# Performance work log

Measured on AMD Instinct MI355X. Metric: run time of the kernel, lower is better.

## Reference

```python
import jax, jax.numpy as jnp
import numpy as np

N = 100000          # nodes
E = 1600000         # edges (avg degree 16)
IN_DIM = 128
OUT_DIM = 128
H = 4               # num_heads
D = OUT_DIM // H    # per-head dim = 32
R = 64              # num relations
NEG_SLOPE = 0.2     # DGL GATConv default


def setup_inputs() -> dict:
    key = jax.random.key(0)
    ks = jax.random.split(key, 9)
    h = jax.random.normal(ks[0], (N, IN_DIM), dtype=jnp.float32)
    src = jax.random.randint(ks[1], (E,), 0, N, dtype=jnp.int32)
    dst = jax.random.randint(ks[2], (E,), 0, N, dtype=jnp.int32)
    rel_types = jax.random.randint(ks[3], (E,), 0, R, dtype=jnp.int32)
    # learned params (GATConv fc weight, attention vectors, bias; relation embedding)
    W = jax.random.normal(ks[4], (H * D, IN_DIM), dtype=jnp.float32) * 0.1
    attn_l = jax.random.normal(ks[5], (H, D), dtype=jnp.float32) * 0.1
    attn_r = jax.random.normal(ks[6], (H, D), dtype=jnp.float32) * 0.1
    bias = jax.random.normal(ks[7], (H * D,), dtype=jnp.float32) * 0.01
    rel_emb = jax.random.normal(ks[8], (R, IN_DIM), dtype=jnp.float32) * 0.1
    return {"h": h, "src": src, "dst": dst, "rel_types": rel_types,
            "W": W, "attn_l": attn_l, "attn_r": attn_r, "bias": bias,
            "rel_emb": rel_emb}


def reference(h, src, dst, rel_types, W, attn_l, attn_r, bias, rel_emb):
    # NOTE: the original module builds edata 'e' = h[src] + rel_emb[rel_types],
    # but DGL's GATConv never reads it, so it does not affect the output.
    # Eval mode: feat_drop / attn_drop disabled (deterministic reference).

    # GATConv: project and split heads. [N, H, D]
    feat = (h @ W.T).reshape(N, H, D)
    # per-node attention logits: a_l^T Wh_i, a_r^T Wh_j  -> [N, H]
    el = (feat * attn_l).sum(-1)
    er = (feat * attn_r).sum(-1)
    # per-edge score e_ij = LeakyReLU(el[src] + er[dst])  -> [E, H]
    e = jax.nn.leaky_relu(el[src] + er[dst], NEG_SLOPE)
    # segment softmax over incoming edges of each destination node
    m = jax.ops.segment_max(e, dst, num_segments=N)           # [N, H]
    a = jnp.exp(e - m[dst])                                    # [E, H]
    denom = jax.ops.segment_sum(a, dst, num_segments=N)       # [N, H]
    alpha = a / denom[dst]                                     # [E, H]
    # weighted scatter-aggregate of source features
    msg = feat[src] * alpha[:, :, None]                        # [E, H, D]
    out = jax.ops.segment_sum(msg, dst, num_segments=N)       # [N, H, D]
    out = out + bias.reshape(1, H, D)
    # mean over heads -> [N, D]
    return out.mean(axis=1)
```

## Files before the change

### kernel.cpp

```cpp
#include <hip/hip_runtime.h>
#include <hip/hip_bf16.h>
#include <math.h>

#define NEG_SLOPE 0.2f

__device__ __forceinline__ float bf2f(unsigned int hw) {
    return __uint_as_float(hw << 16);
}
__device__ __forceinline__ unsigned short f2bf(float f) {
    unsigned int u = __float_as_uint(f);
    u += 0x7FFFu + ((u >> 16) & 1u);
    return (unsigned short)(u >> 16);
}

__global__ __launch_bounds__(256, 3) void k_gemm(const float* __restrict__ h,
                                                 const float* __restrict__ W,
                                                 unsigned short* __restrict__ featp,
                                                 int N) {
    __shared__ float As[64 * 68];
    __shared__ float Bs[128 * 64];
    const int tid = threadIdx.x;
    const int rb = blockIdx.x * 64;
    const int tc = tid & 31;
    const int tr = tid >> 5;

    float acc[8][4];
#pragma unroll
    for (int i = 0; i < 8; ++i)
#pragma unroll
        for (int j = 0; j < 4; ++j) acc[i][j] = 0.0f;

    for (int kch = 0; kch < 2; ++kch) {
        if (kch) __syncthreads();
#pragma unroll
        for (int i = 0; i < 4; ++i) {
            int chunk = i * 256 + tid;
            int r = chunk >> 4;
            int kc = (chunk & 15) << 2;
            int row = rb + r;
            float4 v = make_float4(0.f, 0.f, 0.f, 0.f);
            if (row < N) v = *(const float4*)(h + (size_t)row * 128 + kch * 64 + kc);
            *(float4*)(As + r * 68 + kc) = v;
        }
#pragma unroll
        for (int i = 0; i < 8; ++i) {
            int chunk = i * 256 + tid;
            int c = chunk >> 4;
            int kc = (chunk & 15) << 2;
            float4 v = *(const float4*)(W + (size_t)c * 128 + kch * 64 + kc);
            int slot = (kc >> 2) ^ (c & 7);
            *(float4*)(Bs + (c << 6) + (slot << 2)) = v;
        }
        __syncthreads();

#pragma unroll 4
        for (int k4 = 0; k4 < 64; k4 += 4) {
            float4 b[4];
#pragma unroll
            for (int j = 0; j < 4; ++j) {
                int c = tc + 32 * j;
                int slot = (k4 >> 2) ^ (c & 7);
                b[j] = *(const float4*)(Bs + (c << 6) + (slot << 2));
            }
            float4 a[8];
#pragma unroll
            for (int i = 0; i < 8; ++i)
                a[i] = *(const float4*)(As + (tr * 8 + i) * 68 + k4);
#pragma unroll
            for (int i = 0; i < 8; ++i)
#pragma unroll
                for (int j = 0; j < 4; ++j)
                    acc[i][j] += a[i].x * b[j].x + a[i].y * b[j].y +
                                 a[i].z * b[j].z + a[i].w * b[j].w;
        }
    }
#pragma unroll
    for (int i = 0; i < 8; ++i) {
        int row = rb + tr * 8 + i;
        if (row < N) {
            ushort4 pk;
            pk.x = f2bf(acc[i][0]);
            pk.y = f2bf(acc[i][1]);
            pk.z = f2bf(acc[i][2]);
            pk.w = f2bf(acc[i][3]);
            *(ushort4*)(featp + (size_t)row * 128 + tc * 4) = pk;
        }
    }
}

__global__ void k_elr(const unsigned short* __restrict__ featp,
                      const float* __restrict__ attn_l,
                      const float* __restrict__ attn_r,
                      float* __restrict__ el, float* __restrict__ er, int N) {
    int g = blockIdx.x * blockDim.x + threadIdx.x;
    int node = g >> 5;
    int d = g & 31;
    if (node >= N) return;
    uint2 u = *(const uint2*)(featp + (size_t)node * 128 + d * 4);
    float f0 = bf2f(u.x & 0xffffu);
    float f1 = bf2f(u.x >> 16);
    float f2 = bf2f(u.y & 0xffffu);
    float f3 = bf2f(u.y >> 16);
    float pl0 = f0 * attn_l[d],      pr0 = f0 * attn_r[d];
    float pl1 = f1 * attn_l[32 + d], pr1 = f1 * attn_r[32 + d];
    float pl2 = f2 * attn_l[64 + d], pr2 = f2 * attn_r[64 + d];
    float pl3 = f3 * attn_l[96 + d], pr3 = f3 * attn_r[96 + d];
#pragma unroll
    for (int m = 1; m < 32; m <<= 1) {
        pl0 += __shfl_xor(pl0, m); pr0 += __shfl_xor(pr0, m);
        pl1 += __shfl_xor(pl1, m); pr1 += __shfl_xor(pr1, m);
        pl2 += __shfl_xor(pl2, m); pr2 += __shfl_xor(pr2, m);
        pl3 += __shfl_xor(pl3, m); pr3 += __shfl_xor(pr3, m);
    }
    if (d == 0) {
        *(float4*)(el + (size_t)node * 4) = make_float4(pl0, pl1, pl2, pl3);
        *(float4*)(er + (size_t)node * 4) = make_float4(pr0, pr1, pr2, pr3);
    }
}

__global__ void k_hist(const int* __restrict__ dst, int* __restrict__ cnt,
                       int* __restrict__ pos, int E) {
    int e = blockIdx.x * blockDim.x + threadIdx.x;
    if (e < E) pos[e] = atomicAdd(&cnt[dst[e]], 1);
}

__global__ void k_scan1(const int* __restrict__ cnt, int* __restrict__ bsum, int N) {
    __shared__ int sd[256];
    int t = threadIdx.x;
    int i = blockIdx.x * 256 + t;
    sd[t] = (i < N) ? cnt[i] : 0;
    __syncthreads();
    for (int s = 128; s > 0; s >>= 1) {
        if (t < s) sd[t] += sd[t + s];
        __syncthreads();
    }
    if (t == 0) bsum[blockIdx.x] = sd[0];
}

__global__ void k_scan2(int* __restrict__ bsum, int nb) {
    __shared__ int sd[1024];
    int t = threadIdx.x;
    sd[t] = (t < nb) ? bsum[t] : 0;
    __syncthreads();
    for (int off = 1; off < 1024; off <<= 1) {
        int add = (t >= off) ? sd[t - off] : 0;
        __syncthreads();
        sd[t] += add;
        __syncthreads();
    }
    if (t < nb) bsum[t] = (t == 0) ? 0 : sd[t - 1];
}

__global__ void k_scan3(const int* __restrict__ cnt, const int* __restrict__ bsum,
                        int* __restrict__ row, int N) {
    __shared__ int sd[256];
    int t = threadIdx.x;
    int i = blockIdx.x * 256 + t;
    int v = (i < N) ? cnt[i] : 0;
    sd[t] = v;
    __syncthreads();
    for (int off = 1; off < 256; off <<= 1) {
        int add = (t >= off) ? sd[t - off] : 0;
        __syncthreads();
        sd[t] += add;
        __syncthreads();
    }
    if (i < N) row[i] = bsum[blockIdx.x] + sd[t] - v;
}

__global__ void k_scatter(const int* __restrict__ src, const int* __restrict__ dst,
                          const int* __restrict__ pos, const int* __restrict__ row,
                          int* __restrict__ esrc, int E) {
    int e = blockIdx.x * blockDim.x + threadIdx.x;
    if (e < E) esrc[row[dst[e]] + pos[e]] = src[e];
}

__global__ __launch_bounds__(256) void k_pull(const int* __restrict__ esrc,
                                              const int* __restrict__ row,
                                              const int* __restrict__ cnt,
                                              const float* __restrict__ el,
                                              const float* __restrict__ er,
                                              const unsigned short* __restrict__ featp,
                                              const float* __restrict__ bias,
                                              float* __restrict__ out, int N) {
    int wave = (int)((blockIdx.x * (size_t)blockDim.x + threadIdx.x) >> 6);
    if (wave >= N) return;
    int lane = threadIdx.x & 63;
    int half = lane >> 5;
    int d = lane & 31;
    int start = row[wave];
    int deg = cnt[wave];
    float4 r4 = *(const float4*)(er + 4 * (size_t)wave);

    float acc0 = 0.f, acc1 = 0.f, acc2 = 0.f, acc3 = 0.f;
    float dn0 = 0.f, dn1 = 0.f, dn2 = 0.f, dn3 = 0.f;

    int s = (half < deg) ? esrc[start + half] : 0;
    for (int i = half; i < deg; i += 2) {
        int s_next = (i + 2 < deg) ? esrc[start + i + 2] : 0;
        float4 l4 = *(const float4*)(el + 4 * (size_t)s);
        uint2 u = *(const uint2*)(featp + (size_t)s * 128 + d * 4);
        float f0 = bf2f(u.x & 0xffffu);
        float f1 = bf2f(u.x >> 16);
        float f2 = bf2f(u.y & 0xffffu);
        float f3 = bf2f(u.y >> 16);
        float v0 = l4.x + r4.x; v0 = v0 > 0.f ? v0 : NEG_SLOPE * v0;
        float v1 = l4.y + r4.y; v1 = v1 > 0.f ? v1 : NEG_SLOPE * v1;
        float v2 = l4.z + r4.z; v2 = v2 > 0.f ? v2 : NEG_SLOPE * v2;
        float v3 = l4.w + r4.w; v3 = v3 > 0.f ? v3 : NEG_SLOPE * v3;
        float a0 = __expf(v0), a1 = __expf(v1), a2 = __expf(v2), a3 = __expf(v3);
        dn0 += a0; dn1 += a1; dn2 += a2; dn3 += a3;
        acc0 += a0 * f0; acc1 += a1 * f1; acc2 += a2 * f2; acc3 += a3 * f3;
        s = s_next;
    }
    acc0 += __shfl_xor(acc0, 32); acc1 += __shfl_xor(acc1, 32);
    acc2 += __shfl_xor(acc2, 32); acc3 += __shfl_xor(acc3, 32);
    dn0 += __shfl_xor(dn0, 32);   dn1 += __shfl_xor(dn1, 32);
    dn2 += __shfl_xor(dn2, 32);   dn3 += __shfl_xor(dn3, 32);

    if (half == 0) {
        float m = 0.f;
        if (dn0 > 0.f)
            m = acc0 / dn0 + acc1 / dn1 + acc2 / dn2 + acc3 / dn3;
        float b = 0.25f * (bias[d] + bias[32 + d] + bias[64 + d] + bias[96 + d]);
        out[(size_t)wave * 32 + d] = 0.25f * m + b;
    }
}

extern "C" void kernel_launch(void* const* d_in, const int* in_sizes, int n_in,
                              void* d_out, int out_size, void* d_ws, size_t ws_size,
                              hipStream_t stream) {
    const float* h      = (const float*)d_in[0];
    const int*   src    = (const int*)d_in[1];
    const int*   dst    = (const int*)d_in[2];
    const float* W      = (const float*)d_in[4];
    const float* attn_l = (const float*)d_in[5];
    const float* attn_r = (const float*)d_in[6];
    const float* bias   = (const float*)d_in[7];
    float* out = (float*)d_out;

    const int N = in_sizes[0] / 128;
    const int E = in_sizes[1];

    float* el = (float*)d_ws;
    float* er = el + (size_t)N * 4;
    unsigned short* featp = (unsigned short*)(er + (size_t)N * 4);
    int* cnt  = (int*)(featp + (size_t)N * 128);
    int* row  = cnt + N;
    int* bsum = row + N;
    int* pos  = bsum + 1024;
    int* esrc = pos + E;
    int nb = (N + 255) / 256;

    k_gemm<<<(N + 63) / 64, 256, 0, stream>>>(h, W, featp, N);
    k_elr<<<((size_t)N * 32 + 255) / 256, 256, 0, stream>>>(featp, attn_l, attn_r,
                                                            el, er, N);
    hipMemsetAsync(cnt, 0, (size_t)N * 4, stream);
    k_hist<<<(E + 255) / 256, 256, 0, stream>>>(dst, cnt, pos, E);
    k_scan1<<<nb, 256, 0, stream>>>(cnt, bsum, N);
    k_scan2<<<1, 1024, 0, stream>>>(bsum, nb);
    k_scan3<<<nb, 256, 0, stream>>>(cnt, bsum, row, N);
    k_scatter<<<(E + 255) / 256, 256, 0, stream>>>(src, dst, pos, row, esrc, E);
    k_pull<<<((size_t)N * 64 + 255) / 256, 256, 0, stream>>>(esrc, row, cnt, el, er,
                                                             featp, bias, out, N);
}
```

Baseline: 407.4 us.

## Fuse independent kernels via block ranges and cooperate on edge scores in pull

The GEMM and the histogram now share one launch, with the histogram in extra blocks that each handle two edges per thread. The scatter and the per-node attention logit computation also share one launch. In the pull kernel, each lane now computes the edge score and exp for one edge per chunk of 64, and the results are broadcast by shuffle for the feature gather. This removes the duplicated per-half exp work and the serial el loads. Fewer launches and overlap of independent work are the goals, at the cost of extra shuffles and a wider reduction of the denominators.

```diff
diff --git a/kernel.cpp b/kernel.cpp
--- a/kernel.cpp
+++ b/kernel.cpp
@@ -1,24 +1,34 @@
 #include <hip/hip_runtime.h>
-#include <hip/hip_bf16.h>
 #include <math.h>
 
 #define NEG_SLOPE 0.2f
 
-__device__ __forceinline__ float bf2f(unsigned int hw) {
+static __device__ __forceinline__ float bf2f(unsigned int hw) {
     return __uint_as_float(hw << 16);
 }
-__device__ __forceinline__ unsigned short f2bf(float f) {
+static __device__ __forceinline__ unsigned short f2bf(float f) {
     unsigned int u = __float_as_uint(f);
     u += 0x7FFFu + ((u >> 16) & 1u);
     return (unsigned short)(u >> 16);
 }
 
-__global__ __launch_bounds__(256, 3) void k_gemm(const float* __restrict__ h,
-                                                 const float* __restrict__ W,
-                                                 unsigned short* __restrict__ featp,
-                                                 int N) {
+__global__ __launch_bounds__(256, 3) void k_gemm_hist(
+    const float* __restrict__ h, const float* __restrict__ W,
+    unsigned short* __restrict__ featp, int N,
+    const int* __restrict__ dst, int* __restrict__ cnt, int* __restrict__ pos,
+    int E, int gemm_blocks)
+{
     __shared__ float As[64 * 68];
     __shared__ float Bs[128 * 64];
+
+    if (blockIdx.x >= gemm_blocks) {
+        int e = (blockIdx.x - gemm_blocks) * 512 + threadIdx.x;
+        if (e < E) pos[e] = atomicAdd(&cnt[dst[e]], 1);
+        e += 256;
+        if (e < E) pos[e] = atomicAdd(&cnt[dst[e]], 1);
+        return;
+    }
+
     const int tid = threadIdx.x;
     const int rb = blockIdx.x * 64;
     const int tc = tid & 31;
@@ -88,11 +98,65 @@
     }
 }
 
-__global__ void k_elr(const unsigned short* __restrict__ featp,
-                      const float* __restrict__ attn_l,
-                      const float* __restrict__ attn_r,
-                      float* __restrict__ el, float* __restrict__ er, int N) {
-    int g = blockIdx.x * blockDim.x + threadIdx.x;
+__global__ void k_scan1(const int* __restrict__ cnt, int* __restrict__ bsum, int N) {
+    __shared__ int sd[256];
+    int t = threadIdx.x;
+    int i = blockIdx.x * 256 + t;
+    sd[t] = (i < N) ? cnt[i] : 0;
+    __syncthreads();
+    for (int s = 128; s > 0; s >>= 1) {
+        if (t < s) sd[t] += sd[t + s];
+        __syncthreads();
+    }
+    if (t == 0) bsum[blockIdx.x] = sd[0];
+}
+
+__global__ void k_scan2(int* __restrict__ bsum, int nb) {
+    __shared__ int sd[1024];
+    int t = threadIdx.x;
+    sd[t] = (t < nb) ? bsum[t] : 0;
+    __syncthreads();
+    for (int off = 1; off < 1024; off <<= 1) {
+        int add = (t >= off) ? sd[t - off] : 0;
+        __syncthreads();
+        sd[t] += add;
+        __syncthreads();
+    }
+    if (t < nb) bsum[t] = (t == 0) ? 0 : sd[t - 1];
+}
+
+__global__ void k_scan3(const int* __restrict__ cnt, const int* __restrict__ bsum,
+                        int* __restrict__ row, int N) {
+    __shared__ int sd[256];
+    int t = threadIdx.x;
+    int i = blockIdx.x * 256 + t;
+    int v = (i < N) ? cnt[i] : 0;
+    sd[t] = v;
+    __syncthreads();
+    for (int off = 1; off < 256; off <<= 1) {
+        int add = (t >= off) ? sd[t - off] : 0;
+        __syncthreads();
+        sd[t] += add;
+        __syncthreads();
+    }
+    if (i < N) row[i] = bsum[blockIdx.x] + sd[t] - v;
+}
+
+__global__ void k_scatter_elr(const int* __restrict__ src, const int* __restrict__ dst,
+                              const int* __restrict__ pos, const int* __restrict__ row,
+                              int* __restrict__ esrc, int E, int scat_blocks,
+                              const unsigned short* __restrict__ featp,
+                              const float* __restrict__ attn_l,
+                              const float* __restrict__ attn_r,
+                              float* __restrict__ el, float* __restrict__ er, int N) {
+    if (blockIdx.x < scat_blocks) {
+        int e = blockIdx.x * 512 + threadIdx.x;
+        if (e < E) esrc[row[dst[e]] + pos[e]] = src[e];
+        e += 256;
+        if (e < E) esrc[row[dst[e]] + pos[e]] = src[e];
+        return;
+    }
+    int g = (blockIdx.x - scat_blocks) * 256 + threadIdx.x;
     int node = g >> 5;
     int d = g & 31;
     if (node >= N) return;
@@ -116,63 +180,6 @@
         *(float4*)(el + (size_t)node * 4) = make_float4(pl0, pl1, pl2, pl3);
         *(float4*)(er + (size_t)node * 4) = make_float4(pr0, pr1, pr2, pr3);
     }
-}
-
-__global__ void k_hist(const int* __restrict__ dst, int* __restrict__ cnt,
-                       int* __restrict__ pos, int E) {
-    int e = blockIdx.x * blockDim.x + threadIdx.x;
-    if (e < E) pos[e] = atomicAdd(&cnt[dst[e]], 1);
-}
-
-__global__ void k_scan1(const int* __restrict__ cnt, int* __restrict__ bsum, int N) {
-    __shared__ int sd[256];
-    int t = threadIdx.x;
-    int i = blockIdx.x * 256 + t;
-    sd[t] = (i < N) ? cnt[i] : 0;
-    __syncthreads();
-    for (int s = 128; s > 0; s >>= 1) {
-        if (t < s) sd[t] += sd[t + s];
-        __syncthreads();
-    }
-    if (t == 0) bsum[blockIdx.x] = sd[0];
-}
-
-__global__ void k_scan2(int* __restrict__ bsum, int nb) {
-    __shared__ int sd[1024];
-    int t = threadIdx.x;
-    sd[t] = (t < nb) ? bsum[t] : 0;
-    __syncthreads();
-    for (int off = 1; off < 1024; off <<= 1) {
-        int add = (t >= off) ? sd[t - off] : 0;
-        __syncthreads();
-        sd[t] += add;
-        __syncthreads();
-    }
-    if (t < nb) bsum[t] = (t == 0) ? 0 : sd[t - 1];
-}
-
-__global__ void k_scan3(const int* __restrict__ cnt, const int* __restrict__ bsum,
-                        int* __restrict__ row, int N) {
-    __shared__ int sd[256];
-    int t = threadIdx.x;
-    int i = blockIdx.x * 256 + t;
-    int v = (i < N) ? cnt[i] : 0;
-    sd[t] = v;
-    __syncthreads();
-    for (int off = 1; off < 256; off <<= 1) {
-        int add = (t >= off) ? sd[t - off] : 0;
-        __syncthreads();
-        sd[t] += add;
-        __syncthreads();
-    }
-    if (i < N) row[i] = bsum[blockIdx.x] + sd[t] - v;
-}
-
-__global__ void k_scatter(const int* __restrict__ src, const int* __restrict__ dst,
-                          const int* __restrict__ pos, const int* __restrict__ row,
-                          int* __restrict__ esrc, int E) {
-    int e = blockIdx.x * blockDim.x + threadIdx.x;
-    if (e < E) esrc[row[dst[e]] + pos[e]] = src[e];
 }
 
 __global__ __launch_bounds__(256) void k_pull(const int* __restrict__ esrc,
@@ -195,35 +202,49 @@
     float acc0 = 0.f, acc1 = 0.f, acc2 = 0.f, acc3 = 0.f;
     float dn0 = 0.f, dn1 = 0.f, dn2 = 0.f, dn3 = 0.f;
 
-    int s = (half < deg) ? esrc[start + half] : 0;
-    for (int i = half; i < deg; i += 2) {
-        int s_next = (i + 2 < deg) ? esrc[start + i + 2] : 0;
-        float4 l4 = *(const float4*)(el + 4 * (size_t)s);
-        uint2 u = *(const uint2*)(featp + (size_t)s * 128 + d * 4);
-        float f0 = bf2f(u.x & 0xffffu);
-        float f1 = bf2f(u.x >> 16);
-        float f2 = bf2f(u.y & 0xffffu);
-        float f3 = bf2f(u.y >> 16);
-        float v0 = l4.x + r4.x; v0 = v0 > 0.f ? v0 : NEG_SLOPE * v0;
-        float v1 = l4.y + r4.y; v1 = v1 > 0.f ? v1 : NEG_SLOPE * v1;
-        float v2 = l4.z + r4.z; v2 = v2 > 0.f ? v2 : NEG_SLOPE * v2;
-        float v3 = l4.w + r4.w; v3 = v3 > 0.f ? v3 : NEG_SLOPE * v3;
-        float a0 = __expf(v0), a1 = __expf(v1), a2 = __expf(v2), a3 = __expf(v3);
-        dn0 += a0; dn1 += a1; dn2 += a2; dn3 += a3;
-        acc0 += a0 * f0; acc1 += a1 * f1; acc2 += a2 * f2; acc3 += a3 * f3;
-        s = s_next;
+    for (int base = 0; base < deg; base += 64) {
+        int m = deg - base;
+        if (m > 64) m = 64;
+        int s_mine = 0;
+        float a0 = 0.f, a1 = 0.f, a2 = 0.f, a3 = 0.f;
+        if (lane < m) {
+            s_mine = esrc[start + base + lane];
+            float4 l4 = *(const float4*)(el + 4 * (size_t)s_mine);
+            float v0 = l4.x + r4.x; v0 = v0 > 0.f ? v0 : NEG_SLOPE * v0;
+            float v1 = l4.y + r4.y; v1 = v1 > 0.f ? v1 : NEG_SLOPE * v1;
+            float v2 = l4.z + r4.z; v2 = v2 > 0.f ? v2 : NEG_SLOPE * v2;
+            float v3 = l4.w + r4.w; v3 = v3 > 0.f ? v3 : NEG_SLOPE * v3;
+            a0 = __expf(v0); a1 = __expf(v1); a2 = __expf(v2); a3 = __expf(v3);
+            dn0 += a0; dn1 += a1; dn2 += a2; dn3 += a3;
+        }
+        for (int ii = 0; ii < m; ii += 2) {
+            int i = ii + half;
+            int sj   = __shfl(s_mine, i);
+            float b0 = __shfl(a0, i);
+            float b1 = __shfl(a1, i);
+            float b2 = __shfl(a2, i);
+            float b3 = __shfl(a3, i);
+            uint2 u = *(const uint2*)(featp + (size_t)sj * 128 + d * 4);
+            float f0 = bf2f(u.x & 0xffffu);
+            float f1 = bf2f(u.x >> 16);
+            float f2 = bf2f(u.y & 0xffffu);
+            float f3 = bf2f(u.y >> 16);
+            acc0 += b0 * f0; acc1 += b1 * f1; acc2 += b2 * f2; acc3 += b3 * f3;
+        }
     }
     acc0 += __shfl_xor(acc0, 32); acc1 += __shfl_xor(acc1, 32);
     acc2 += __shfl_xor(acc2, 32); acc3 += __shfl_xor(acc3, 32);
-    dn0 += __shfl_xor(dn0, 32);   dn1 += __shfl_xor(dn1, 32);
-    dn2 += __shfl_xor(dn2, 32);   dn3 += __shfl_xor(dn3, 32);
-
+#pragma unroll
+    for (int m = 1; m < 64; m <<= 1) {
+        dn0 += __shfl_xor(dn0, m); dn1 += __shfl_xor(dn1, m);
+        dn2 += __shfl_xor(dn2, m); dn3 += __shfl_xor(dn3, m);
+    }
     if (half == 0) {
-        float m = 0.f;
+        float msum = 0.f;
         if (dn0 > 0.f)
-            m = acc0 / dn0 + acc1 / dn1 + acc2 / dn2 + acc3 / dn3;
+            msum = acc0 / dn0 + acc1 / dn1 + acc2 / dn2 + acc3 / dn3;
         float b = 0.25f * (bias[d] + bias[32 + d] + bias[64 + d] + bias[96 + d]);
-        out[(size_t)wave * 32 + d] = 0.25f * m + b;
+        out[(size_t)wave * 32 + d] = 0.25f * msum + b;
     }
 }
 
@@ -252,15 +273,23 @@
     int* esrc = pos + E;
     int nb = (N + 255) / 256;
 
-    k_gemm<<<(N + 63) / 64, 256, 0, stream>>>(h, W, featp, N);
-    k_elr<<<((size_t)N * 32 + 255) / 256, 256, 0, stream>>>(featp, attn_l, attn_r,
-                                                            el, er, N);
     hipMemsetAsync(cnt, 0, (size_t)N * 4, stream);
-    k_hist<<<(E + 255) / 256, 256, 0, stream>>>(dst, cnt, pos, E);
+
+    int gemm_blocks = (N + 63) / 64;
+    int hist_blocks = (E + 511) / 512;
+    k_gemm_hist<<<gemm_blocks + hist_blocks, 256, 0, stream>>>(
+        h, W, featp, N, dst, cnt, pos, E, gemm_blocks);
+
     k_scan1<<<nb, 256, 0, stream>>>(cnt, bsum, N);
     k_scan2<<<1, 1024, 0, stream>>>(bsum, nb);
     k_scan3<<<nb, 256, 0, stream>>>(cnt, bsum, row, N);
-    k_scatter<<<(E + 255) / 256, 256, 0, stream>>>(src, dst, pos, row, esrc, E);
+
+    int scat_blocks = (E + 511) / 512;
+    int elr_blocks = ((size_t)N * 32 + 255) / 256;
+    k_scatter_elr<<<scat_blocks + elr_blocks, 256, 0, stream>>>(
+        src, dst, pos, row, esrc, E, scat_blocks,
+        featp, attn_l, attn_r, el, er, N);
+
     k_pull<<<((size_t)N * 64 + 255) / 256, 256, 0, stream>>>(esrc, row, cnt, el, er,
                                                              featp, bias, out, N);
 }
```

Result: faster. 351.4 us (-13.7%).
